# Optimization experiments

Measured on AMD Instinct MI355X. Metric: run time of the kernel, lower is better.

## Reference

```python
import jax, jax.numpy as jnp
import numpy as np

OBS, PRED = 8, 12
EIN, EHID, NOISE = 64, 256, 64
GEMB = 64
DHID = EHID + NOISE  # 320
G, NPER = 8, 192
B = G * NPER


def leaky(x):
    return jnp.where(x > 0, x, 0.2 * x)


def lstm_cell(x, h, c, Wih, Whh, bih, bhh):
    gates = x @ Wih.T + bih + h @ Whh.T + bhh
    i, f, g, o = jnp.split(gates, 4, axis=-1)
    c = jax.nn.sigmoid(f) * c + jax.nn.sigmoid(i) * jnp.tanh(g)
    h = jax.nn.sigmoid(o) * jnp.tanh(c)
    return h, c


def kmeans(x, k, niter=10):
    # deterministic init: first k points (torch used randperm)
    c = x[:k]
    ar = jnp.arange(k)
    for _ in range(niter):
        d2 = ((x[:, None, :] - c[None, :, :]) ** 2).sum(-1)  # [N,k]
        a = jnp.argmin(d2, axis=1)
        onehot = (a[:, None] == ar[None, :]).astype(x.dtype)  # [N,k]
        cnt = onehot.sum(0)
        mean = (onehot.T @ x) / jnp.maximum(cnt, 1.0)[:, None]
        c = jnp.where((cnt == 0)[:, None], x[:k], mean)  # reseed dead clusters
    d2 = ((x[:, None, :] - c[None, :, :]) ** 2).sum(-1)
    return jnp.argmin(d2, axis=1)


def signed_graph(node, W_ne, b_ne, W_att, b_att):
    n, D = node.shape
    emb = node @ W_ne.T + b_ne  # [n,E]
    E = emb.shape[1]
    a_other, a_self = W_att[0, :E], W_att[0, E:]
    # e[i,j] = a_other.emb[j] + a_self.emb[i] + b  (cat([other, self]) order)
    e = (emb @ a_other)[None, :] + (emb @ a_self)[:, None] + b_att[0]
    edge = jax.nn.softmax(leaky(e), axis=0)
    edge = jnp.triu(edge, 0) + jnp.triu(edge, 1).T  # symmetrize from upper tri
    d = edge.sum(1)
    L = jnp.diag(d) - edge
    dinv = 1.0 / jnp.sqrt(d)
    L_sym = dinv[:, None] * L * dinv[None, :]
    lam, H = jnp.linalg.eigh(jax.lax.stop_gradient(L_sym))  # ascending eigvals
    H = H[:, :2]  # two smallest
    Hn = H / jnp.sqrt((H ** 2).sum(1, keepdims=True))
    labels = kmeans(Hn, int(np.ceil(n / 2)))
    same = labels[:, None] == labels[None, :]
    NEG = jnp.float32(-1e8)
    pos_alpha = jax.nn.softmax(leaky(edge * jnp.where(same, 1.0, NEG)), axis=0)
    neg_alpha = jax.nn.softmax(leaky(edge * jnp.where(same, NEG, 1.0)), axis=0)
    feat = jax.nn.relu(pos_alpha[..., None] * node[None, :, :]) + \
           jax.nn.relu(neg_alpha[..., None] * node[None, :, :])  # [n,n,D]
    return feat.sum(axis=1)


def setup_inputs():
    key = jax.random.key(0)
    ks = jax.random.split(key, 22)
    p = lambda k, s: jax.random.normal(k, s, jnp.float32) * 0.1
    starts = jnp.arange(G, dtype=jnp.int32) * NPER
    return {
        "input_traj": jax.random.normal(ks[0], (OBS + PRED, B, 2), jnp.float32),
        "enc_h0": jax.random.normal(ks[1], (B, EHID), jnp.float32),
        "enc_c0": jax.random.normal(ks[2], (B, EHID), jnp.float32),
        "noise_z": jax.random.normal(ks[3], (G, NOISE), jnp.float32),
        "W_emb": p(ks[4], (EIN, 2)), "b_emb": p(ks[5], (EIN,)),
        "Wih_e": p(ks[6], (4 * EHID, EIN)), "Whh_e": p(ks[7], (4 * EHID, EHID)),
        "bih_e": p(ks[8], (4 * EHID,)), "bhh_e": p(ks[9], (4 * EHID,)),
        "Wih_d": p(ks[10], (4 * DHID, EIN)), "Whh_d": p(ks[11], (4 * DHID, DHID)),
        "bih_d": p(ks[12], (4 * DHID,)), "bhh_d": p(ks[13], (4 * DHID,)),
        "W_out": p(ks[14], (2, DHID)), "b_out": p(ks[15], (2,)),
        "W_ne": p(ks[16], (GEMB, DHID)), "b_ne": p(ks[17], (GEMB,)),
        "W_att": p(ks[18], (1, 2 * GEMB)), "b_att": p(ks[19], (1,)),
        "seq_start_end": jnp.stack([starts, starts + NPER], axis=1),
    }


def reference(input_traj, enc_h0, enc_c0, noise_z, W_emb, b_emb,
              Wih_e, Whh_e, bih_e, bhh_e, Wih_d, Whh_d, bih_d, bhh_d,
              W_out, b_out, W_ne, b_ne, W_att, b_att, seq_start_end):
    # ---- encoder ----
    x = jax.nn.relu(input_traj @ W_emb.T + b_emb)  # [T,B,EIN]
    def step(carry, xt):
        h, c = carry
        h, c = lstm_cell(xt, h, c, Wih_e, Whh_e, bih_e, bhh_e)
        return (h, c), None
    (h_enc, _), _ = jax.lax.scan(step, (enc_h0, enc_c0), x[:OBS])
    # ---- add per-scene noise (equal-sized scenes) ----
    z = jnp.repeat(noise_z, NPER, axis=0)  # [B,NOISE]
    h = jnp.concatenate([h_enc, z], axis=1)  # [B,DHID]
    c = jnp.zeros_like(h)
    traj_out = input_traj[OBS - 1]  # [B,2]
    sg = jax.vmap(lambda nd: signed_graph(nd, W_ne, b_ne, W_att, b_att))
    preds = []
    for i in range(PRED):  # eval mode: no teacher forcing
        inp = jax.nn.relu(traj_out @ W_emb.T + b_emb)
        if i % 12 == 4:
            h = sg(h.reshape(G, NPER, DHID)).reshape(B, DHID)
        h, c = lstm_cell(inp, h, c, Wih_d, Whh_d, bih_d, bhh_d)
        traj_out = h @ W_out.T + b_out
        preds.append(traj_out)
    return jnp.stack(preds)  # [PRED,B,2]
```

## Files before the change

### kernel.cpp

```cpp
#include <hip/hip_runtime.h>
#include <hip/hip_bf16.h>

typedef __hip_bfloat16 bf16;

#define NN 192
#define NG 8
#define BB 1536
#define EHID 256
#define DH 320
#define PRED 12
#define STRD 192
#define ATILE (NN*STRD)

__device__ __forceinline__ int aoffc(int r, int c){
  int c4 = c >> 2;
  int s = (c4 & ~7) | ((c4 + 3*r) & 7);
  return r*STRD + (s << 2) + (c & 3);
}

#define WAVE_SYNC() do { asm volatile("" ::: "memory"); __builtin_amdgcn_wave_barrier(); } while (0)

__device__ __forceinline__ float waveSum(float v){
#pragma unroll
  for (int o = 32; o > 0; o >>= 1) v += __shfl_down(v, o);
  return v;
}
__device__ __forceinline__ double waveSumD(double v){
#pragma unroll
  for (int o = 32; o > 0; o >>= 1) v += __shfl_down(v, o);
  return v;
}
__device__ __forceinline__ float waveAllSum(float v){
#pragma unroll
  for (int o = 32; o > 0; o >>= 1) v += __shfl_xor(v, o);
  return v;
}
__device__ __forceinline__ double waveAllSumD(double v){
#pragma unroll
  for (int o = 32; o > 0; o >>= 1) v += __shfl_xor(v, o);
  return v;
}

__device__ __forceinline__ double blockSumD(double v, double* red){
  int lane = threadIdx.x & 63, wid = threadIdx.x >> 6, nw = (int)blockDim.x >> 6;
  double s = waveSumD(v);
  __syncthreads();
  if (lane == 0) red[wid] = s;
  __syncthreads();
  if (wid == 0){
    double t = (lane < nw) ? red[lane] : 0.0;
    t = waveSumD(t);
    if (lane == 0) red[0] = t;
  }
  __syncthreads();
  return red[0];
}


__global__ void k_zero_int(int* __restrict__ p, int n){
  int i = blockIdx.x*blockDim.x + threadIdx.x;
  if (i < n) p[i] = 0;
}
__global__ void k_zero_f(float* __restrict__ p, int n){
  int i = blockIdx.x*blockDim.x + threadIdx.x;
  if (i < n) p[i] = 0.f;
}

__global__ void k_probe(const unsigned short* __restrict__ src, int n, int* __restrict__ cnt){
  int tid = blockIdx.x*blockDim.x + threadIdx.x;
  int stride = gridDim.x*blockDim.x;
  int bad = 0;
  for (int j = tid; j < n; j += stride){
    float v = __uint_as_float(((unsigned int)src[j]) << 16);
    if (!(fabsf(v) < 100.f)) bad++;
  }
#pragma unroll
  for (int o = 32; o > 0; o >>= 1) bad += __shfl_down(bad, o);
  if ((threadIdx.x & 63) == 0 && bad > 0) atomicAdd(cnt, bad);
}
__global__ void k_flag(const int* __restrict__ cnt, int* __restrict__ flag){
  *flag = (*cnt > 4096) ? 1 : 0;
}

struct CvtArgs {
  const void* src[20];
  float*      dst[20];
  int         n[20];
};

__global__ void k_convert(CvtArgs a, const int* __restrict__ flag){
  int id = blockIdx.y;
  int n = a.n[id];
  float* d = a.dst[id];
  int t = blockIdx.x*blockDim.x + threadIdx.x;
  int stride = gridDim.x*blockDim.x;
  if (*flag == 0){
    const bf16* s = (const bf16*)a.src[id];
    for (int j = t; j < n; j += stride) d[j] = __bfloat162float(s[j]);
  } else {
    const float* s = (const float*)a.src[id];
    for (int j = t; j < n; j += stride) d[j] = s[j];
  }
}

__global__ void k_permw(const void* __restrict__ src, float* __restrict__ dst,
                        int H, int K, const int* __restrict__ flag){
  int idx = blockIdx.x*blockDim.x + threadIdx.x;
  int n = 4*H*K;
  if (idx >= n) return;
  int r = idx / K, kk = idx - r*K;
  int j = r >> 2, q = r & 3;
  int si = (q*H + j)*K + kk;
  float v;
  if (*flag == 0) v = __bfloat162float(((const bf16*)src)[si]);
  else            v = ((const float*)src)[si];
  dst[idx] = v;
}

__global__ void k_permb(const void* __restrict__ b1, const void* __restrict__ b2,
                        float* __restrict__ dst, int H, const int* __restrict__ flag){
  int r = blockIdx.x*blockDim.x + threadIdx.x;
  if (r >= 4*H) return;
  int j = r >> 2, q = r & 3;
  int si = q*H + j;
  float v1, v2;
  if (*flag == 0){
    v1 = __bfloat162float(((const bf16*)b1)[si]);
    v2 = __bfloat162float(((const bf16*)b2)[si]);
  } else {
    v1 = ((const float*)b1)[si];
    v2 = ((const float*)b2)[si];
  }
  dst[r] = v1 + v2;
}


__global__ void k_concat(const float* __restrict__ henc, const float* __restrict__ z,
                         float* __restrict__ h){
  int idx = blockIdx.x*blockDim.x + threadIdx.x;
  if (idx >= BB*DH) return;
  int b = idx / DH, j = idx - b*DH;
  h[idx] = (j < EHID) ? henc[b*EHID + j] : z[(b/NN)*64 + (j - EHID)];
}

__global__ void k_copy_f(const float* __restrict__ in, float* __restrict__ dst, int n){
  int i = blockIdx.x*blockDim.x + threadIdx.x;
  if (i < n) dst[i] = in[i];
}

__global__ __launch_bounds__(256) void k_gates_lstm(
    const float* __restrict__ traj2,
    const float* __restrict__ Wemb, const float* __restrict__ bemb,
    const float* __restrict__ Wp, const float* __restrict__ Up,
    const float* __restrict__ bsum,
    const float* __restrict__ hin, float* __restrict__ hout,
    float* __restrict__ cst, int H){
  __shared__ __align__(16) float inpT[64][68];
  __shared__ __align__(16) float As[32][68];
  __shared__ __align__(16) float Ws[32][68];
  int tid = threadIdx.x;
  int tx = tid & 15, ty = tid >> 4;
  int n0 = blockIdx.x * 64, m0 = blockIdx.y * 64;

  {
    int r = tid & 63;
    float x = traj2[(size_t)(m0 + r)*2];
    float y = traj2[(size_t)(m0 + r)*2 + 1];
    for (int e = tid >> 6; e < 64; e += 4){
      float v = Wemb[e*2]*x + Wemb[e*2+1]*y + bemb[e];
      inpT[e][r] = v > 0.f ? v : 0.f;
    }
  }
  float acc[4][4] = {};
  for (int k0 = 0; k0 < 64; k0 += 32){
    {
      int am = tid >> 2, ak = (tid & 3) * 8;
      const float* srcW = Wp + (size_t)(n0+am)*64 + k0 + ak;
      float4 w0 = *(const float4*)(srcW);
      float4 w1 = *(const float4*)(srcW+4);
      Ws[ak+0][am]=w0.x; Ws[ak+1][am]=w0.y; Ws[ak+2][am]=w0.z; Ws[ak+3][am]=w0.w;
      Ws[ak+4][am]=w1.x; Ws[ak+5][am]=w1.y; Ws[ak+6][am]=w1.z; Ws[ak+7][am]=w1.w;
    }
    __syncthreads();
#pragma unroll
    for (int k = 0; k < 32; ++k){
      float4 a0 = *(const float4*)&inpT[k0+k][ty*4];
      float4 b0 = *(const float4*)&Ws[k][tx*4];
      float av[4] = {a0.x, a0.y, a0.z, a0.w};
      float bv[4] = {b0.x, b0.y, b0.z, b0.w};
#pragma unroll
      for (int i = 0; i < 4; ++i)
#pragma unroll
        for (int j = 0; j < 4; ++j)
          acc[i][j] += av[i]*bv[j];
    }
    __syncthreads();
  }
  for (int k0 = 0; k0 < H; k0 += 32){
    {
      int am = tid >> 2, ak = (tid & 3) * 8;
      const float* srcA = hin + (size_t)(m0+am)*H + k0 + ak;
      float4 f0 = *(const float4*)(srcA);
      float4 f1 = *(const float4*)(srcA+4);
      As[ak+0][am]=f0.x; As[ak+1][am]=f0.y; As[ak+2][am]=f0.z; As[ak+3][am]=f0.w;
      As[ak+4][am]=f1.x; As[ak+5][am]=f1.y; As[ak+6][am]=f1.z; As[ak+7][am]=f1.w;
      const float* srcW = Up + (size_t)(n0+am)*H + k0 + ak;
      float4 w0 = *(const float4*)(srcW);
      float4 w1 = *(const float4*)(srcW+4);
      Ws[ak+0][am]=w0.x; Ws[ak+1][am]=w0.y; Ws[ak+2][am]=w0.z; Ws[ak+3][am]=w0.w;
      Ws[ak+4][am]=w1.x; Ws[ak+5][am]=w1.y; Ws[ak+6][am]=w1.z; Ws[ak+7][am]=w1.w;
    }
    __syncthreads();
#pragma unroll
    for (int k = 0; k < 32; ++k){
      float4 a0 = *(const float4*)&As[k][ty*4];
      float4 b0 = *(const float4*)&Ws[k][tx*4];
      float av[4] = {a0.x, a0.y, a0.z, a0.w};
      float bv[4] = {b0.x, b0.y, b0.z, b0.w};
#pragma unroll
      for (int i = 0; i < 4; ++i)
#pragma unroll
        for (int j = 0; j < 4; ++j)
          acc[i][j] += av[i]*bv[j];
    }
    __syncthreads();
  }
  int s = (n0 >> 2) + tx;
  float4 bq = *(const float4*)&bsum[n0 + tx*4];
#pragma unroll
  for (int i2 = 0; i2 < 4; ++i2){
    int row = m0 + ty*4 + i2;
    float gi = acc[i2][0] + bq.x;
    float gf = acc[i2][1] + bq.y;
    float gg = acc[i2][2] + bq.z;
    float go = acc[i2][3] + bq.w;
    float si = 1.f/(1.f+expf(-gi));
    float sf = 1.f/(1.f+expf(-gf));
    float so = 1.f/(1.f+expf(-go));
    size_t cidx = (size_t)row*H + s;
    float cc = sf*cst[cidx] + si*tanhf(gg);
    cst[cidx] = cc;
    hout[cidx] = so*tanhf(cc);
  }
}

__global__ void k_outproj(const float* __restrict__ h, const float* __restrict__ W,
                          const float* __restrict__ bo, float* __restrict__ traj,
                          void* __restrict__ outbase, int step, const int* __restrict__ flag){
  int b = blockIdx.x, lane = threadIdx.x;
  const float* hb = h + (size_t)b*DH;
  float a0 = 0.f, a1 = 0.f;
  for (int k = lane; k < DH; k += 64){
    float hv = hb[k];
    a0 += hv*W[k];
    a1 += hv*W[DH+k];
  }
  a0 = waveSum(a0); a1 = waveSum(a1);
  if (lane == 0){
    a0 += bo[0]; a1 += bo[1];
    traj[b*2] = a0; traj[b*2+1] = a1;
    size_t idx = (size_t)step*BB*2 + (size_t)b*2;
    if (*flag == 0){
      bf16* o = (bf16*)outbase;
      o[idx] = __float2bfloat16(a0); o[idx+1] = __float2bfloat16(a1);
    } else {
      float* o = (float*)outbase;
      o[idx] = a0; o[idx+1] = a1;
    }
  }
}


__global__ void k_sg_emb(const float* __restrict__ h, const float* __restrict__ Wne,
                         const float* __restrict__ bne, const float* __restrict__ Watt,
                         double* __restrict__ sself, double* __restrict__ sother){
  int node = blockIdx.x, e = threadIdx.x;
  const float* hb = h + (size_t)node*DH;
  double acc = (double)bne[e];
  for (int k = 0; k < DH; ++k) acc += (double)hb[k]*(double)Wne[e*DH+k];
  double po = acc * (double)Watt[e];
  double ps = acc * (double)Watt[64+e];
  po = waveSumD(po); ps = waveSumD(ps);
  if (e == 0){ sother[node] = po; sself[node] = ps; }
}

__global__ void k_sg_edgecol(const double* __restrict__ sself, const double* __restrict__ sother,
                             const float* __restrict__ batt, double* __restrict__ edge){
  int g = blockIdx.x, j = threadIdx.x;
  const double* ss = sself + g*NN;
  double bb = (double)batt[0];
  double sj = sother[g*NN + j];
  double m = -1e300;
  for (int i = 0; i < NN; ++i){
    double e = ss[i] + sj + bb; e = e > 0.0 ? e : 0.2*e;
    m = fmax(m, e);
  }
  double sum = 0.0;
  for (int i = 0; i < NN; ++i){
    double e = ss[i] + sj + bb; e = e > 0.0 ? e : 0.2*e;
    sum += exp(e - m);
  }
  double* E = edge + (size_t)g*NN*NN;
  for (int i = 0; i < NN; ++i){
    double e = ss[i] + sj + bb; e = e > 0.0 ? e : 0.2*e;
    E[i*NN + j] = exp(e - m)/sum;
  }
}

__global__ void k_sg_sym(const double* __restrict__ edge, double* __restrict__ esym){
  int idx = blockIdx.x*blockDim.x + threadIdx.x;
  if (idx >= NG*NN*NN) return;
  int g = idx / (NN*NN), r = idx - g*NN*NN;
  int i = r / NN, j = r - i*NN;
  const double* E = edge + (size_t)g*NN*NN;
  esym[idx] = (i <= j) ? E[i*NN + j] : E[j*NN + i];
}

__global__ void k_sg_dsum(const double* __restrict__ esym, double* __restrict__ darr){
  int i = blockIdx.x*blockDim.x + threadIdx.x;
  if (i >= NG*NN) return;
  int g = i / NN, li = i - g*NN;
  const double* E = esym + (size_t)g*NN*NN + (size_t)li*NN;
  double s = 0.0;
  for (int j = 0; j < NN; ++j) s += E[j];
  darr[i] = fmax(s, 1e-300);
}

__global__ void k_sg_lsym(const double* __restrict__ esym, const double* __restrict__ darr,
                          float* __restrict__ Afull){
  int idx = blockIdx.x*blockDim.x + threadIdx.x;
  if (idx >= NG*NN*NN) return;
  int g = idx / (NN*NN), r = idx - g*NN*NN;
  int i = r / NN, j = r - i*NN;
  double w = esym[idx];
  double lij = (i == j) ? (darr[g*NN+i] - w) : (-w);
  Afull[(size_t)g*ATILE + aoffc(i, j)] =
      (float)(lij / (sqrt(darr[g*NN+i])*sqrt(darr[g*NN+j])));
}

__global__ __launch_bounds__(1024) void k_sg_eigen(const float* __restrict__ Afull,
                                                   const double* __restrict__ darr,
                                                   double* __restrict__ v1out){
  extern __shared__ unsigned char ldsraw[];
  float*  A     = (float*)ldsraw;
  double* dd    = (double*)(ldsraw + 147456);
  double* ee    = dd + NN;
  double* yv    = ee + NN;
  double* lu_d  = yv + NN;
  double* lu_du = lu_d + NN;
  double* lu_du2= lu_du + NN;
  double* redA  = lu_du2 + NN;
  double* redB  = redA + 16;
  double* salpha= redB + 16;
  float*  uu    = (float*)(ldsraw + 156944);
  float*  ww    = uu + NN;
  int*    lu_piv= (int*)(ww + NN);
  float*  pp4   = (float*)yv;
  double* lu_dl = (double*)uu;

  int g = blockIdx.x, tid = threadIdx.x;
  int lane = tid & 63, wid = tid >> 6;
  int rtid = tid & 255, team = tid >> 8;

  const float* src = Afull + (size_t)g*ATILE;
  for (int t = tid*4; t < ATILE; t += 4096) *(float4*)&A[t] = *(const float4*)&src[t];
  __syncthreads();

  for (int k = 0; k < NN-65; ++k){
    int m = NN-1-k;
    int i = k+1+rtid;
    float x = 0.f;
    if (rtid < m) x = A[aoffc(i, k)];
    if (tid == 0) *salpha = (double)x;
    if (team == 0){
      float part = (rtid > 0 && rtid < m) ? x*x : 0.f;
      part = waveSum(part);
      if (lane == 0) redA[wid] = (double)part;
    }
    __syncthreads();
    double sigma = redA[0] + redA[1] + redA[2] + redA[3];
    double alpha = *salpha;
    double beta, tau, scale;
    if (sigma <= 1e-30){ tau = 0.0; beta = alpha; scale = 0.0; }
    else {
      beta = -copysign(sqrt(alpha*alpha + sigma), alpha);
      tau = (beta - alpha)/beta;
      scale = 1.0/(alpha - beta);
    }
    float tau_f = (float)tau, scale_f = (float)scale;
    if (tid == 0){
      dd[k] = (double)A[aoffc(k, k)];
      ee[k] = beta;
      A[aoffc(k, k)] = tau_f;
    }
    if (tau != 0.0){
      float u_i = 0.f;
      if (rtid < m) u_i = (rtid == 0) ? 1.f : x*scale_f;
      if (team == 0 && rtid < m){
        uu[i] = u_i;
        if (rtid >= 1) A[aoffc(i, k)] = u_i;
      }
      __syncthreads();
      int c0 = k+1;
      int cA = (c0+3)&~3;
      int cB = (c0+31)&~31;
      int NB = (NN - cB) >> 5;
      const int rb = i*STRD;
      const int rk3 = (3*i) & 7;
      int off[8];
#pragma unroll
      for (int j = 0; j < 8; ++j) off[j] = ((j + rk3) & 7) << 2;
      if (rtid < m){
        float s0=0.f, s1=0.f, s2=0.f, s3=0.f, accs=0.f;
        if (team == 3){
          int c = c0;
          for (; c < cA; ++c) accs += A[aoffc(i, c)]*uu[c];
          for (; c < cB; c += 4){
            int c4 = c>>2; int s = (c4&~7)|((c4+rk3)&7);
            float4 a4 = *(const float4*)&A[rb + (s<<2)];
            float4 u4 = *(const float4*)&uu[c];
            s0 += a4.x*u4.x; s1 += a4.y*u4.y; s2 += a4.z*u4.z; s3 += a4.w*u4.w;
          }
        }
        for (int b = team; b < NB; b += 4){
          int c = cB + (b<<5);
          const int cb = rb + c;
#pragma unroll
          for (int j = 0; j < 8; ++j){
            float4 a4 = *(const float4*)&A[cb + off[j]];
            float4 u4 = *(const float4*)&uu[c + 4*j];
            s0 += a4.x*u4.x; s1 += a4.y*u4.y; s2 += a4.z*u4.z; s3 += a4.w*u4.w;
          }
        }
        pp4[team*NN + i] = ((s0+s1)+(s2+s3)) + accs;
      }
      __syncthreads();
      float p = 0.f;
      if (rtid < m)
        p = tau_f*(pp4[i] + pp4[NN + i] + pp4[2*NN + i] + pp4[3*NN + i]);
      if (team == 0){
        float vp = (rtid < m) ? u_i*p : 0.f;
        vp = waveSum(vp);
        if (lane == 0) redB[wid] = (double)vp;
      }
      __syncthreads();
      double vtp = redB[0] + redB[1] + redB[2] + redB[3];
      float Kc_f = (float)(0.5*tau*vtp);
      float w_i = 0.f;
      if (rtid < m){
        w_i = p - Kc_f*u_i;
        if (team == 0) ww[i] = w_i;
      }
      __syncthreads();
      if (rtid < m){
        if (team == 3){
          int c = c0;
          for (; c < cA; ++c) A[aoffc(i, c)] -= u_i*ww[c] + w_i*uu[c];
          for (; c < cB; c += 4){
            int c4 = c>>2; int s = (c4&~7)|((c4+rk3)&7);
            float* ap = &A[rb + (s<<2)];
            float4 a4 = *(const float4*)ap;
            float4 u4 = *(const float4*)&uu[c];
            float4 w4 = *(const float4*)&ww[c];
            a4.x -= u_i*w4.x + w_i*u4.x;
            a4.y -= u_i*w4.y + w_i*u4.y;
            a4.z -= u_i*w4.z + w_i*u4.z;
            a4.w -= u_i*w4.w + w_i*u4.w;
            *(float4*)ap = a4;
          }
        }
        for (int b = team; b < NB; b += 4){
          int c = cB + (b<<5);
          const int cb = rb + c;
#pragma unroll
          for (int j = 0; j < 8; ++j){
            float* ap = &A[cb + off[j]];
            float4 a4 = *(const float4*)ap;
            float4 u4 = *(const float4*)&uu[c + 4*j];
            float4 w4 = *(const float4*)&ww[c + 4*j];
            a4.x -= u_i*w4.x + w_i*u4.x;
            a4.y -= u_i*w4.y + w_i*u4.y;
            a4.z -= u_i*w4.z + w_i*u4.z;
            a4.w -= u_i*w4.w + w_i*u4.w;
            *(float4*)ap = a4;
          }
        }
      }
      __syncthreads();
    } else {
      __syncthreads();
    }
  }

  if (wid != 0) return;

  for (int k = NN-65; k < NN-2; ++k){
    int m = NN-1-k;
    int i = k+1+lane;
    bool act = lane < m;
    float x = act ? A[aoffc(i, k)] : 0.f;
    float part = (lane > 0) ? x*x : 0.f;
    float sig_f = waveAllSum(part);
    float alpha_f = __shfl(x, 0);
    double sigma = (double)sig_f;
    double alpha = (double)alpha_f;
    double beta, tau, scale;
    if (sigma <= 1e-30){ tau = 0.0; beta = alpha; scale = 0.0; }
    else {
      beta = -copysign(sqrt(alpha*alpha + sigma), alpha);
      tau = (beta - alpha)/beta;
      scale = 1.0/(alpha - beta);
    }
    float tau_f = (float)tau, scale_f = (float)scale;
    if (lane == 0){
      dd[k] = (double)A[aoffc(k, k)];
      ee[k] = beta;
      A[aoffc(k, k)] = tau_f;
    }
    if (tau == 0.0) continue;
    float u = (lane == 0) ? 1.f : x*scale_f;
    int base4 = (k+1) & ~3;
    int ph = (k+1) - base4;
    uu[lane + ph] = u;
    if (lane >= 1 && act) A[aoffc(i, k)] = u;
    WAVE_SYNC();
    int ic = act ? i : (k+1);
    const int rb = ic*STRD;
    const int rk3 = (3*ic) & 7;
    float s0=0.f, s1=0.f, s2=0.f, s3=0.f, accs=0.f;
    {
      int c = k+1;
      int cA = (c+3)&~3; if (cA > NN) cA = NN;
      for (; c < cA; ++c) accs += A[aoffc(ic, c)]*uu[c-base4];
      for (; c < NN; c += 4){
        int c4 = c>>2; int s = (c4&~7)|((c4+rk3)&7);
        float4 a4 = *(const float4*)&A[rb + (s<<2)];
        float4 u4 = *(const float4*)&uu[c-base4];
        s0 += a4.x*u4.x; s1 += a4.y*u4.y; s2 += a4.z*u4.z; s3 += a4.w*u4.w;
      }
    }
    float p = tau_f*(((s0+s1)+(s2+s3)) + accs);
    float vtp = waveAllSum(u*p);
    float Kc_f = (float)(0.5*tau*(double)vtp);
    float w = p - Kc_f*u;
    ww[lane + ph] = w;
    WAVE_SYNC();
    if (act){
      int c = k+1;
      int cA = (c+3)&~3; if (cA > NN) cA = NN;
      for (; c < cA; ++c) A[aoffc(i, c)] -= u*ww[c-base4] + w*uu[c-base4];
      for (; c < NN; c += 4){
        int c4 = c>>2; int s = (c4&~7)|((c4+rk3)&7);
        float* ap = &A[rb + (s<<2)];
        float4 a4 = *(const float4*)ap;
        float4 u4 = *(const float4*)&uu[c-base4];
        float4 w4 = *(const float4*)&ww[c-base4];
        a4.x -= u*w4.x + w*u4.x;
        a4.y -= u*w4.y + w*u4.y;
        a4.z -= u*w4.z + w*u4.z;
        a4.w -= u*w4.w + w*u4.w;
        *(float4*)ap = a4;
      }
    }
    WAVE_SYNC();
  }

  if (lane == 0){
    dd[NN-2] = (double)A[aoffc(NN-2, NN-2)];
    ee[NN-2] = (double)A[aoffc(NN-1, NN-2)];
    dd[NN-1] = (double)A[aoffc(NN-1, NN-1)];
  }
  WAVE_SYNC();

  {
    double mn = 1e300, mx = -1e300;
    for (int i = lane; i < NN; i += 64){
      double r = (i > 0 ? fabs(ee[i-1]) : 0.0) + (i < NN-1 ? fabs(ee[i]) : 0.0);
      mn = fmin(mn, dd[i]-r); mx = fmax(mx, dd[i]+r);
    }
#pragma unroll
    for (int o = 32; o > 0; o >>= 1){
      mn = fmin(mn, __shfl_down(mn, o));
      mx = fmax(mx, __shfl_down(mx, o));
    }
    mn = __shfl(mn, 0); mx = __shfl(mx, 0);
    double lo = mn - 1e-8 - 1e-9*fabs(mn);
    double hi = mx + 1e-8 + 1e-9*fabs(mx);
    for (int it = 0; it < 10; ++it){
      double lam = lo + (hi-lo)*((double)(lane+1)/65.0);
      int cnt = 0;
      double q = dd[0] - lam;
      if (q < 0.0) cnt++;
      for (int i2 = 1; i2 < NN; ++i2){
        double den = q;
        if (fabs(den) < 1e-280) den = (den < 0.0) ? -1e-280 : 1e-280;
        q = dd[i2] - lam - ee[i2-1]*ee[i2-1]/den;
        if (q < 0.0) cnt++;
      }
      unsigned long long bal = __ballot(cnt >= 2);
      if (bal == 0ull){
        lo = lo + (hi-lo)*(64.0/65.0);
      } else {
        int j0 = __ffsll(bal) - 1;
        double nl = lo + (hi-lo)*((double)j0/65.0);
        double nh = lo + (hi-lo)*((double)(j0+1)/65.0);
        lo = nl; hi = nh;
      }
    }
    double lam1 = 0.5*(lo+hi);

    if (lane == 0){
      for (int i = 0; i < NN; ++i) lu_d[i] = dd[i] - lam1;
      for (int i = 0; i < NN-1; ++i){ lu_dl[i] = ee[i]; lu_du[i] = ee[i]; }
      for (int i = 0; i < NN-2; ++i) lu_du2[i] = 0.0;
      for (int i = 0; i < NN-1; ++i){
        if (fabs(lu_d[i]) >= fabs(lu_dl[i])){
          double di = lu_d[i];
          if (fabs(di) < 1e-30){ di = (di < 0.0) ? -1e-30 : 1e-30; lu_d[i] = di; }
          double fact = lu_dl[i]/di;
          lu_dl[i] = fact;
          lu_d[i+1] -= fact*lu_du[i];
          lu_piv[i] = 0;
        } else {
          double fact = lu_d[i]/lu_dl[i];
          lu_d[i] = lu_dl[i];
          double tmp = lu_d[i+1];
          lu_d[i+1] = lu_du[i] - fact*tmp;
          if (i < NN-2){ lu_du2[i] = lu_du[i+1]; lu_du[i+1] = -fact*lu_du[i+1]; }
          lu_du[i] = tmp;
          lu_dl[i] = fact;
          lu_piv[i] = 1;
        }
      }
      if (fabs(lu_d[NN-1]) < 1e-30)
        lu_d[NN-1] = (lu_d[NN-1] < 0.0) ? -1e-30 : 1e-30;
      for (int i = 0; i < NN; ++i) yv[i] = 1.0 + 0.001*(double)((i*37)%29);
      for (int round = 0; round < 2; ++round){
        for (int i = 0; i < NN-1; ++i){
          if (lu_piv[i] == 0){
            yv[i+1] -= lu_dl[i]*yv[i];
          } else {
            double t = yv[i]; yv[i] = yv[i+1]; yv[i+1] = t - lu_dl[i]*yv[i];
          }
        }
        double mx1 = 0.0;
        for (int i = 0; i < NN; ++i) mx1 = fmax(mx1, fabs(yv[i]));
        double inv1 = (mx1 > 0.0 && isfinite(mx1)) ? 1.0/mx1 : 1.0;
        for (int i = 0; i < NN; ++i) yv[i] *= inv1;
        yv[NN-1] = yv[NN-1]/lu_d[NN-1];
        yv[NN-2] = (yv[NN-2] - lu_du[NN-2]*yv[NN-1])/lu_d[NN-2];
        for (int i = NN-3; i >= 0; --i)
          yv[i] = (yv[i] - lu_du[i]*yv[i+1] - lu_du2[i]*yv[i+2])/lu_d[i];
        double mxv = 0.0;
        for (int i = 0; i < NN; ++i) mxv = fmax(mxv, fabs(yv[i]));
        double inv = (mxv > 0.0 && isfinite(mxv)) ? 1.0/mxv : 1.0;
        for (int i = 0; i < NN; ++i){
          double val = yv[i]*inv;
          if (!isfinite(val)) val = 0.0;
          yv[i] = val;
        }
      }
    }
  }
  WAVE_SYNC();

  {
    int r0 = lane, r1 = lane+64, r2 = lane+128;
    double y0 = yv[r0], y1 = yv[r1], y2 = yv[r2];
    for (int k = NN-3; k >= 0; --k){
      double tau = (double)A[aoffc(k, k)];
      if (tau != 0.0){
        double u0 = (r0 > k) ? ((r0 == k+1) ? 1.0 : (double)A[aoffc(r0, k)]) : 0.0;
        double u1 = (r1 > k) ? ((r1 == k+1) ? 1.0 : (double)A[aoffc(r1, k)]) : 0.0;
        double u2 = (r2 > k) ? ((r2 == k+1) ? 1.0 : (double)A[aoffc(r2, k)]) : 0.0;
        double part = u0*y0 + u1*y1 + u2*y2;
        part = waveAllSumD(part);
        double s = tau*part;
        y0 -= s*u0; y1 -= s*u1; y2 -= s*u2;
      }
    }

    const double* dg = darr + (size_t)g*NN;
    double d0 = dg[r0], d1 = dg[r1], d2 = dg[r2];
    double sd0 = sqrt(d0), sd1 = sqrt(d1), sd2 = sqrt(d2);
    double pd  = waveAllSumD(sd0*y0 + sd1*y1 + sd2*y2);
    double pn2 = waveAllSumD(d0 + d1 + d2);
    double coef = pd/fmax(pn2, 1e-300);
    y0 -= coef*sd0; y1 -= coef*sd1; y2 -= coef*sd2;
    double s2 = waveAllSumD(y0*y0 + y1*y1 + y2*y2);
    double nrm = sqrt(s2);
    double inv = (nrm > 0.0 && isfinite(nrm)) ? 1.0/nrm : 0.0;
    double o0 = y0*inv, o1 = y1*inv, o2 = y2*inv;
    if (!isfinite(o0)) o0 = 0.0;
    if (!isfinite(o1)) o1 = 0.0;
    if (!isfinite(o2)) o2 = 0.0;
    v1out[g*NN + r0] = o0;
    v1out[g*NN + r1] = o1;
    v1out[g*NN + r2] = o2;
  }
}

__global__ __launch_bounds__(256) void k_sg_kmeans(const double* __restrict__ darr,
                                                   const double* __restrict__ v1,
                                                   int* __restrict__ labels){
  __shared__ double px[NN], py[NN], cx[96], cy[96];
  __shared__ int lab[NN];
  __shared__ double red[16];
  int g = blockIdx.x, tid = threadIdx.x;
  double part = 0.0;
  for (int i = tid; i < NN; i += 256) part += darr[g*NN + i];
  double sumd = blockSumD(part, red);
  double invn = 1.0/sqrt(fmax(sumd, 1e-300));
  for (int i = tid; i < NN; i += 256){
    double h0 = sqrt(darr[g*NN + i])*invn;
    double h1 = v1[g*NN + i];
    double rn = sqrt(h0*h0 + h1*h1);
    double ax = h0/rn, ay = h1/rn;
    if (!isfinite(ax)) ax = 0.0;
    if (!isfinite(ay)) ay = 0.0;
    px[i] = ax; py[i] = ay;
  }
  __syncthreads();
  if (tid < 96){ cx[tid] = px[tid]; cy[tid] = py[tid]; }
  __syncthreads();
  for (int it = 0; it <= 10; ++it){
    if (tid < NN){
      double bx = px[tid], by = py[tid];
      double best = 1e300; int bi = 0;
      for (int a = 0; a < 96; ++a){
        double dx = bx - cx[a], dy = by - cy[a];
        double d2 = dx*dx + dy*dy;
        if (d2 < best){ best = d2; bi = a; }
      }
      lab[tid] = bi;
    }
    __syncthreads();
    if (it == 10) break;
    if (tid < 96){
      int c = 0; double sx = 0.0, sy = 0.0;
      for (int i = 0; i < NN; ++i){
        if (lab[i] == tid){ c++; sx += px[i]; sy += py[i]; }
      }
      if (c > 0){ cx[tid] = sx/(double)c; cy[tid] = sy/(double)c; }
      else      { cx[tid] = px[tid];      cy[tid] = py[tid]; }
    }
    __syncthreads();
  }
  if (tid < NN) labels[g*NN + tid] = lab[tid];
}

__global__ void k_sg_alpha(const double* __restrict__ esym, const int* __restrict__ labels,
                           float* __restrict__ S){
  __shared__ int lbs[NN];
  int g = blockIdx.x, j = threadIdx.x;
  if (j < NN) lbs[j] = labels[g*NN + j];
  __syncthreads();
  const double* E = esym + (size_t)g*NN*NN;
  const double NEG = -100000000.0;
  int lj = lbs[j];
  double mp = -1e300, mn = -1e300;
  for (int i = 0; i < NN; ++i){
    double w = E[i*NN + j];
    bool sm = (lbs[i] == lj);
    double vp = sm ? w : w*NEG; vp = vp > 0.0 ? vp : 0.2*vp;
    double vn = sm ? w*NEG : w; vn = vn > 0.0 ? vn : 0.2*vn;
    mp = fmax(mp, vp); mn = fmax(mn, vn);
  }
  double sp = 0.0, sn = 0.0;
  for (int i = 0; i < NN; ++i){
    double w = E[i*NN + j];
    bool sm = (lbs[i] == lj);
    double vp = sm ? w : w*NEG; vp = vp > 0.0 ? vp : 0.2*vp;
    double vn = sm ? w*NEG : w; vn = vn > 0.0 ? vn : 0.2*vn;
    sp += exp(vp - mp); sn += exp(vn - mn);
  }
  float* So = S + (size_t)g*NN*NN;
  for (int i = 0; i < NN; ++i){
    double w = E[i*NN + j];
    bool sm = (lbs[i] == lj);
    double vp = sm ? w : w*NEG; vp = vp > 0.0 ? vp : 0.2*vp;
    double vn = sm ? w*NEG : w; vn = vn > 0.0 ? vn : 0.2*vn;
    So[i*NN + j] = (float)(exp(vp - mp)/sp + exp(vn - mn)/sn);
  }
}

__global__ __launch_bounds__(320) void k_sg_feat(const float* __restrict__ S,
                                                 const float* __restrict__ hin,
                                                 float* __restrict__ hout){
  int r = blockIdx.x;
  int g = r / NN, li = r - g*NN;
  int dh = threadIdx.x;
  const float* Srow = S + (size_t)g*NN*NN + (size_t)li*NN;
  const float* hb = hin + (size_t)g*NN*DH;
  float acc = 0.f;
  for (int j = 0; j < NN; ++j){
    float w = Srow[j];
    float x = hb[(size_t)j*DH + dh];
    acc += w*(x > 0.f ? x : 0.f);
  }
  hout[(size_t)r*DH + dh] = acc;
}


extern "C" void kernel_launch(void* const* d_in, const int* in_sizes, int n_in,
                              void* d_out, int out_size, void* d_ws, size_t ws_size,
                              hipStream_t stream){
  (void)n_in; (void)out_size; (void)ws_size;

  float* ws = (float*)d_ws;
  float* inp   = ws;
  float* gates = ws + 98304;
  float* hA    = ws + 2064384;
  float* hB    = ws + 2555904;
  float* cD    = ws + 3047424;
  float* traj  = ws + 3538944;
  double* sself_d  = (double*)(ws + 3542016);
  double* sother_d = (double*)(ws + 3545088);
  double* darr_d   = (double*)(ws + 3548160);
  double* v1_d     = (double*)(ws + 3551232);
  int*    labels   = (int*)(ws + 3554304);
  double* edge_d = (double*)gates;
  double* esym_d = (double*)(gates + 589824);
  float*  Afull  = gates + 1179648;
  float*  Smat   = gates;
  float*  hC     = gates;
  float* a_traj = ws + 3555840;
  float* a_z    = ws + 3617280;
  float* a_Wemb = ws + 3617792;
  float* a_bemb = ws + 3617920;
  float* a_Wihe = ws + 3617984;
  float* a_Whhe = ws + 3683520;
  float* a_bihe = ws + 3945664;
  float* a_bhhe = ws + 3946688;
  float* a_Wihd = ws + 3947712;
  float* a_Whhd = ws + 4029632;
  float* a_bihd = ws + 4439232;
  float* a_bhhd = ws + 4440512;
  float* a_Wout = ws + 4441792;
  float* a_bout = ws + 4442432;
  float* a_Wne  = ws + 4442496;
  float* a_bne  = ws + 4462976;
  float* a_Watt = ws + 4463040;
  float* a_batt = ws + 4463168;
  int* cnt  = (int*)(ws + 4463232);
  int* flag = (int*)(ws + 4463233);
  (void)inp; (void)a_bhhe; (void)a_bhhd;

  const int EIG_LDS = 159248;
  hipFuncSetAttribute((const void*)k_sg_eigen,
                      hipFuncAttributeMaxDynamicSharedMemorySize, EIG_LDS);

  k_zero_int<<<1, 64, 0, stream>>>(cnt, 2);
  k_probe<<<256, 256, 0, stream>>>((const unsigned short*)d_in[1], in_sizes[1], cnt);
  k_flag<<<1, 1, 0, stream>>>(cnt, flag);

  CvtArgs ca;
  float* dsts[20] = { a_traj, hB, cD, a_z, a_Wemb, a_bemb, a_Wihe, a_Whhe, a_bihe,
                      a_bhhe, a_Wihd, a_Whhd, a_bihd, a_bhhd, a_Wout, a_bout,
                      a_Wne, a_bne, a_Watt, a_batt };
  for (int i = 0; i < 20; ++i){
    ca.src[i] = d_in[i];
    ca.dst[i] = dsts[i];
    ca.n[i]   = in_sizes[i];
  }
  k_convert<<<dim3(512, 20), 256, 0, stream>>>(ca, flag);

  k_permw<<<(4*EHID*64   + 255)/256, 256, 0, stream>>>(d_in[6],  a_Wihe, EHID, 64,   flag);
  k_permw<<<(4*EHID*EHID + 255)/256, 256, 0, stream>>>(d_in[7],  a_Whhe, EHID, EHID, flag);
  k_permb<<<(4*EHID + 255)/256, 256, 0, stream>>>(d_in[8], d_in[9],  a_bihe, EHID, flag);
  k_permw<<<(4*DH*64     + 255)/256, 256, 0, stream>>>(d_in[10], a_Wihd, DH, 64, flag);
  k_permw<<<(4*DH*DH     + 255)/256, 256, 0, stream>>>(d_in[11], a_Whhd, DH, DH, flag);
  k_permb<<<(4*DH + 255)/256, 256, 0, stream>>>(d_in[12], d_in[13], a_bihd, DH, flag);

  float* ecur = hB;
  float* eoth = hC;
  for (int t = 0; t < 8; ++t){
    k_gates_lstm<<<dim3(4*EHID/64, BB/64), 256, 0, stream>>>(
        a_traj + (size_t)t*BB*2, a_Wemb, a_bemb,
        a_Wihe, a_Whhe, a_bihe, ecur, eoth, cD, EHID);
    float* tmp = ecur; ecur = eoth; eoth = tmp;
  }

  k_concat<<<(BB*DH+255)/256, 256, 0, stream>>>(ecur, a_z, hA);
  k_zero_f<<<(BB*DH+255)/256, 256, 0, stream>>>(cD, BB*DH);
  k_copy_f<<<(BB*2+255)/256, 256, 0, stream>>>(a_traj + (size_t)7*BB*2, traj, BB*2);

  float* hcur = hA;
  float* hoth = hB;
  for (int i = 0; i < PRED; ++i){
    if (i == 4){
      k_sg_emb<<<BB, 64, 0, stream>>>(hcur, a_Wne, a_bne, a_Watt, sself_d, sother_d);
      k_sg_edgecol<<<NG, NN, 0, stream>>>(sself_d, sother_d, a_batt, edge_d);
      k_sg_sym<<<(NG*NN*NN+255)/256, 256, 0, stream>>>(edge_d, esym_d);
      k_sg_dsum<<<(NG*NN+255)/256, 256, 0, stream>>>(esym_d, darr_d);
      k_sg_lsym<<<(NG*NN*NN+255)/256, 256, 0, stream>>>(esym_d, darr_d, Afull);
      k_sg_eigen<<<NG, 1024, EIG_LDS, stream>>>(Afull, darr_d, v1_d);
      k_sg_kmeans<<<NG, 256, 0, stream>>>(darr_d, v1_d, labels);
      k_sg_alpha<<<NG, NN, 0, stream>>>(esym_d, labels, Smat);
      k_sg_feat<<<BB, DH, 0, stream>>>(Smat, hcur, hoth);
      float* tmp = hcur; hcur = hoth; hoth = tmp;
    }
    k_gates_lstm<<<dim3(4*DH/64, BB/64), 256, 0, stream>>>(
        traj, a_Wemb, a_bemb,
        a_Wihd, a_Whhd, a_bihd, hcur, hoth, cD, DH);
    { float* tmp = hcur; hcur = hoth; hoth = tmp; }
    k_outproj<<<BB, 64, 0, stream>>>(hcur, a_Wout, a_bout, traj, d_out, i, flag);
  }
}
```

Baseline: 2.265 ms.

## Enlarge LSTM gate GEMM tile to 128 rows and merge eigen-reduction barriers

The fused gates+LSTM kernel now computes a 128x64 output tile per block with 8x4 accumulators per thread. The input embedding is computed per k-chunk into the shared A tile instead of a separate 64x64 buffer. This halves the number of row blocks and doubles reuse of each loaded weight tile, at the cost of more registers and fewer blocks in flight. Separately, in the Householder tridiagonalization, every wave now reduces u·(partial) directly and the partials are summed over 16 waves, which removes one __syncthreads per column step.

```diff
diff --git a/kernel.cpp b/kernel.cpp
--- a/kernel.cpp
+++ b/kernel.cpp
@@ -155,23 +155,20 @@
     const float* __restrict__ bsum,
     const float* __restrict__ hin, float* __restrict__ hout,
     float* __restrict__ cst, int H){
-  __shared__ __align__(16) float inpT[64][68];
-  __shared__ __align__(16) float As[32][68];
+  __shared__ __align__(16) float As[32][132];
   __shared__ __align__(16) float Ws[32][68];
+  __shared__ float xs[128], ys[128];
   int tid = threadIdx.x;
   int tx = tid & 15, ty = tid >> 4;
-  int n0 = blockIdx.x * 64, m0 = blockIdx.y * 64;
-
-  {
-    int r = tid & 63;
-    float x = traj2[(size_t)(m0 + r)*2];
-    float y = traj2[(size_t)(m0 + r)*2 + 1];
-    for (int e = tid >> 6; e < 64; e += 4){
-      float v = Wemb[e*2]*x + Wemb[e*2+1]*y + bemb[e];
-      inpT[e][r] = v > 0.f ? v : 0.f;
-    }
-  }
-  float acc[4][4] = {};
+  int n0 = blockIdx.x * 64, m0 = blockIdx.y * 128;
+
+  if (tid < 128){
+    xs[tid] = traj2[(size_t)(m0 + tid)*2];
+    ys[tid] = traj2[(size_t)(m0 + tid)*2 + 1];
+  }
+  __syncthreads();
+
+  float acc[8][4] = {};
   for (int k0 = 0; k0 < 64; k0 += 32){
     {
       int am = tid >> 2, ak = (tid & 3) * 8;
@@ -181,15 +178,27 @@
       Ws[ak+0][am]=w0.x; Ws[ak+1][am]=w0.y; Ws[ak+2][am]=w0.z; Ws[ak+3][am]=w0.w;
       Ws[ak+4][am]=w1.x; Ws[ak+5][am]=w1.y; Ws[ak+6][am]=w1.z; Ws[ak+7][am]=w1.w;
     }
+    {
+      int r = tid >> 1;
+      int e0 = (tid & 1) * 16;
+      float x = xs[r], y = ys[r];
+#pragma unroll
+      for (int j = 0; j < 16; ++j){
+        int e = k0 + e0 + j;
+        float v = Wemb[e*2]*x + Wemb[e*2+1]*y + bemb[e];
+        As[e0 + j][r] = v > 0.f ? v : 0.f;
+      }
+    }
     __syncthreads();
 #pragma unroll
     for (int k = 0; k < 32; ++k){
-      float4 a0 = *(const float4*)&inpT[k0+k][ty*4];
+      float4 a0 = *(const float4*)&As[k][ty*8];
+      float4 a1 = *(const float4*)&As[k][ty*8+4];
       float4 b0 = *(const float4*)&Ws[k][tx*4];
-      float av[4] = {a0.x, a0.y, a0.z, a0.w};
-      float bv[4] = {b0.x, b0.y, b0.z, b0.w};
-#pragma unroll
-      for (int i = 0; i < 4; ++i)
+      float av[8] = {a0.x,a0.y,a0.z,a0.w,a1.x,a1.y,a1.z,a1.w};
+      float bv[4] = {b0.x,b0.y,b0.z,b0.w};
+#pragma unroll
+      for (int i = 0; i < 8; ++i)
 #pragma unroll
         for (int j = 0; j < 4; ++j)
           acc[i][j] += av[i]*bv[j];
@@ -198,27 +207,33 @@
   }
   for (int k0 = 0; k0 < H; k0 += 32){
     {
-      int am = tid >> 2, ak = (tid & 3) * 8;
+      int am = tid >> 1, ak = (tid & 1) * 16;
       const float* srcA = hin + (size_t)(m0+am)*H + k0 + ak;
       float4 f0 = *(const float4*)(srcA);
       float4 f1 = *(const float4*)(srcA+4);
-      As[ak+0][am]=f0.x; As[ak+1][am]=f0.y; As[ak+2][am]=f0.z; As[ak+3][am]=f0.w;
-      As[ak+4][am]=f1.x; As[ak+5][am]=f1.y; As[ak+6][am]=f1.z; As[ak+7][am]=f1.w;
-      const float* srcW = Up + (size_t)(n0+am)*H + k0 + ak;
+      float4 f2 = *(const float4*)(srcA+8);
+      float4 f3 = *(const float4*)(srcA+12);
+      As[ak+ 0][am]=f0.x; As[ak+ 1][am]=f0.y; As[ak+ 2][am]=f0.z; As[ak+ 3][am]=f0.w;
+      As[ak+ 4][am]=f1.x; As[ak+ 5][am]=f1.y; As[ak+ 6][am]=f1.z; As[ak+ 7][am]=f1.w;
+      As[ak+ 8][am]=f2.x; As[ak+ 9][am]=f2.y; As[ak+10][am]=f2.z; As[ak+11][am]=f2.w;
+      As[ak+12][am]=f3.x; As[ak+13][am]=f3.y; As[ak+14][am]=f3.z; As[ak+15][am]=f3.w;
+      int wm = tid >> 2, wk = (tid & 3) * 8;
+      const float* srcW = Up + (size_t)(n0+wm)*H + k0 + wk;
       float4 w0 = *(const float4*)(srcW);
       float4 w1 = *(const float4*)(srcW+4);
-      Ws[ak+0][am]=w0.x; Ws[ak+1][am]=w0.y; Ws[ak+2][am]=w0.z; Ws[ak+3][am]=w0.w;
-      Ws[ak+4][am]=w1.x; Ws[ak+5][am]=w1.y; Ws[ak+6][am]=w1.z; Ws[ak+7][am]=w1.w;
+      Ws[wk+0][wm]=w0.x; Ws[wk+1][wm]=w0.y; Ws[wk+2][wm]=w0.z; Ws[wk+3][wm]=w0.w;
+      Ws[wk+4][wm]=w1.x; Ws[wk+5][wm]=w1.y; Ws[wk+6][wm]=w1.z; Ws[wk+7][wm]=w1.w;
     }
     __syncthreads();
 #pragma unroll
     for (int k = 0; k < 32; ++k){
-      float4 a0 = *(const float4*)&As[k][ty*4];
+      float4 a0 = *(const float4*)&As[k][ty*8];
+      float4 a1 = *(const float4*)&As[k][ty*8+4];
       float4 b0 = *(const float4*)&Ws[k][tx*4];
-      float av[4] = {a0.x, a0.y, a0.z, a0.w};
-      float bv[4] = {b0.x, b0.y, b0.z, b0.w};
-#pragma unroll
-      for (int i = 0; i < 4; ++i)
+      float av[8] = {a0.x,a0.y,a0.z,a0.w,a1.x,a1.y,a1.z,a1.w};
+      float bv[4] = {b0.x,b0.y,b0.z,b0.w};
+#pragma unroll
+      for (int i = 0; i < 8; ++i)
 #pragma unroll
         for (int j = 0; j < 4; ++j)
           acc[i][j] += av[i]*bv[j];
@@ -228,8 +243,8 @@
   int s = (n0 >> 2) + tx;
   float4 bq = *(const float4*)&bsum[n0 + tx*4];
 #pragma unroll
-  for (int i2 = 0; i2 < 4; ++i2){
-    int row = m0 + ty*4 + i2;
+  for (int i2 = 0; i2 < 8; ++i2){
+    int row = m0 + ty*8 + i2;
     float gi = acc[i2][0] + bq.x;
     float gf = acc[i2][1] + bq.y;
     float gg = acc[i2][2] + bq.z;
@@ -410,6 +425,7 @@
       int off[8];
 #pragma unroll
       for (int j = 0; j < 8; ++j) off[j] = ((j + rk3) & 7) << 2;
+      float sum_t = 0.f;
       if (rtid < m){
         float s0=0.f, s1=0.f, s2=0.f, s3=0.f, accs=0.f;
         if (team == 3){
@@ -432,22 +448,21 @@
             s0 += a4.x*u4.x; s1 += a4.y*u4.y; s2 += a4.z*u4.z; s3 += a4.w*u4.w;
           }
         }
-        pp4[team*NN + i] = ((s0+s1)+(s2+s3)) + accs;
-      }
+        sum_t = ((s0+s1)+(s2+s3)) + accs;
+        pp4[team*NN + i] = sum_t;
+      }
+      float z = (rtid < m) ? u_i*sum_t : 0.f;
+      z = waveSum(z);
+      if (lane == 0) redB[wid] = (double)z;
       __syncthreads();
-      float p = 0.f;
-      if (rtid < m)
-        p = tau_f*(pp4[i] + pp4[NN + i] + pp4[2*NN + i] + pp4[3*NN + i]);
-      if (team == 0){
-        float vp = (rtid < m) ? u_i*p : 0.f;
-        vp = waveSum(vp);
-        if (lane == 0) redB[wid] = (double)vp;
-      }
-      __syncthreads();
-      double vtp = redB[0] + redB[1] + redB[2] + redB[3];
+      double vtpS = 0.0;
+#pragma unroll
+      for (int w = 0; w < 16; ++w) vtpS += redB[w];
+      double vtp = tau*vtpS;
       float Kc_f = (float)(0.5*tau*vtp);
       float w_i = 0.f;
       if (rtid < m){
+        float p = tau_f*(pp4[i] + pp4[NN + i] + pp4[2*NN + i] + pp4[3*NN + i]);
         w_i = p - Kc_f*u_i;
         if (team == 0) ww[i] = w_i;
       }
@@ -875,7 +890,7 @@
   float* ecur = hB;
   float* eoth = hC;
   for (int t = 0; t < 8; ++t){
-    k_gates_lstm<<<dim3(4*EHID/64, BB/64), 256, 0, stream>>>(
+    k_gates_lstm<<<dim3(4*EHID/64, BB/128), 256, 0, stream>>>(
         a_traj + (size_t)t*BB*2, a_Wemb, a_bemb,
         a_Wihe, a_Whhe, a_bihe, ecur, eoth, cD, EHID);
     float* tmp = ecur; ecur = eoth; eoth = tmp;
@@ -900,7 +915,7 @@
       k_sg_feat<<<BB, DH, 0, stream>>>(Smat, hcur, hoth);
       float* tmp = hcur; hcur = hoth; hoth = tmp;
     }
-    k_gates_lstm<<<dim3(4*DH/64, BB/64), 256, 0, stream>>>(
+    k_gates_lstm<<<dim3(4*DH/64, BB/128), 256, 0, stream>>>(
         traj, a_Wemb, a_bemb,
         a_Wihd, a_Whhd, a_bihd, hcur, hoth, cD, DH);
     { float* tmp = hcur; hcur = hoth; hoth = tmp; }
```

Measured after the change: 2.369 ms. 4.6% more time.
